# Kernel optimization log

Hardware: AMD Instinct MI355X
Metric: run time of the kernel (lower is better)

Reference implementation:

```python
import jax, jax.numpy as jnp
import numpy as np

B, T, D, U = 32, 2048, 128, 128


def setup_inputs() -> dict:
    key = jax.random.key(0)
    k1, k2, k3, k4 = jax.random.split(key, 4)
    x = jax.random.normal(k1, (B, T, D), dtype=jnp.float32)
    W_x = jax.random.normal(k2, (D, 4 * U), dtype=jnp.float32) * 0.05
    W_h = jax.random.normal(k3, (U, 4 * U), dtype=jnp.float32) * 0.05
    bias = jax.random.normal(k4, (4 * U,), dtype=jnp.float32) * 0.05
    return {"x": x, "W_x": W_x, "W_h": W_h, "bias": bias}


def reference(x, W_x, W_h, bias):
    # Keras gate order in the packed 4U dim: i, f, c(g), o
    u = W_h.shape[0]
    batch = x.shape[0]
    h0 = jnp.zeros((batch, u), dtype=x.dtype)
    c0 = jnp.zeros((batch, u), dtype=x.dtype)

    def step(carry, x_t):
        h, c = carry
        z = x_t @ W_x + h @ W_h + bias  # [B, 4U], fused 4-gate GEMM
        i = jax.nn.sigmoid(z[:, :u])
        f = jax.nn.sigmoid(z[:, u:2 * u])
        g = jnp.tanh(z[:, 2 * u:3 * u])
        o = jax.nn.sigmoid(z[:, 3 * u:])
        c_new = i * g + f * c
        h_new = o * jnp.tanh(c_new)
        return (h_new, c_new), h_new

    # scan over time: x -> [T, B, D]
    _, hs = jax.lax.scan(step, (h0, c0), jnp.swapaxes(x, 0, 1))
    return hs  # [T, B, U], matches original's np.array(h_sequences)
```

## Files before the change

### kernel.cpp

```cpp
#include <hip/hip_runtime.h>
#include <cstdint>
#include <cstddef>

#define B_ 32
#define T_ 2048
#define D_ 128
#define U_ 128
#define G4_ 512
#define P1_ROWS 32
#define L2E_ 1.4426950408889634f

typedef _Float16 f16x8 __attribute__((ext_vector_type(8)));
typedef _Float16 f16x2 __attribute__((ext_vector_type(2)));
typedef float f32x4 __attribute__((ext_vector_type(4)));

__device__ __forceinline__ void lds_barrier() {
  __builtin_amdgcn_sched_barrier(0);
  asm volatile("s_waitcnt lgkmcnt(0)");
  __builtin_amdgcn_sched_barrier(0);
  __builtin_amdgcn_s_barrier();
  __builtin_amdgcn_sched_barrier(0);
}

__global__ __launch_bounds__(512)
void zx_kernel(const float* __restrict__ x, const float* __restrict__ Wx,
               const float* __restrict__ bias, float* __restrict__ Zx,
               int tbase, int ct) {
  const int j = threadIdx.x;
  const int nt = ct / P1_ROWS;
  const int tblk = blockIdx.x % nt;
  const int b = blockIdx.x / nt;
  const int t0 = tblk * P1_ROWS;
  const float sj = ((j >> 7) == 2) ? (-2.f * L2E_) : (-L2E_);

  __shared__ float xsT[D_ * P1_ROWS];

  const float* xp = x + ((size_t)b * T_ + tbase + t0) * D_;
  {
    int e = j * 8;
    int r = e >> 7;
    int k = e & 127;
    float4 v0 = *(const float4*)(xp + e);
    float4 v1 = *(const float4*)(xp + e + 4);
    xsT[(k + 0) * P1_ROWS + r] = v0.x;
    xsT[(k + 1) * P1_ROWS + r] = v0.y;
    xsT[(k + 2) * P1_ROWS + r] = v0.z;
    xsT[(k + 3) * P1_ROWS + r] = v0.w;
    xsT[(k + 4) * P1_ROWS + r] = v1.x;
    xsT[(k + 5) * P1_ROWS + r] = v1.y;
    xsT[(k + 6) * P1_ROWS + r] = v1.z;
    xsT[(k + 7) * P1_ROWS + r] = v1.w;
  }
  __syncthreads();

  const float bj = bias[j];
  float acc[P1_ROWS];
#pragma unroll
  for (int r = 0; r < P1_ROWS; ++r) acc[r] = bj;

  const float* wp = Wx + j;
  float w = wp[0];
#pragma unroll 2
  for (int k = 0; k < D_; ++k) {
    float wn = (k + 1 < D_) ? wp[(size_t)(k + 1) * G4_] : 0.f;
    const float4* xr = (const float4*)(xsT + k * P1_ROWS);
#pragma unroll
    for (int r4 = 0; r4 < P1_ROWS / 4; ++r4) {
      float4 xv = xr[r4];
      acc[4 * r4 + 0] += xv.x * w;
      acc[4 * r4 + 1] += xv.y * w;
      acc[4 * r4 + 2] += xv.z * w;
      acc[4 * r4 + 3] += xv.w * w;
    }
    w = wn;
  }

  float* zp = Zx + ((size_t)b * G4_ + j) * ct + t0;
#pragma unroll
  for (int q = 0; q < P1_ROWS / 4; ++q)
    ((float4*)zp)[q] = make_float4(sj * acc[4 * q], sj * acc[4 * q + 1],
                                   sj * acc[4 * q + 2], sj * acc[4 * q + 3]);
}

__global__ __launch_bounds__(512)
void lstm_kernel(const float* __restrict__ Zx, const float* __restrict__ Wh,
                 float* __restrict__ out, float* __restrict__ state,
                 int tbase, int ct, int first) {
  const int j = threadIdx.x;
  const int b = blockIdx.x;
  const int w = j >> 6;
  const int lane = j & 63;
  const int l4 = lane & 15;
  const int kg = lane >> 4;
  const int u = w * 16 + l4;

  const bool evn = (kg & 1) == 0;
  const bool lowg = kg < 2;
  const int idx16 = (lane ^ 16) << 2;
  const int idx32 = (lane ^ 32) << 2;
  const float mk = (kg == 2) ? 2.f : 1.f;
  const float bk = (kg == 2) ? -1.f : 0.f;

  f16x8 bf[4][4];
#pragma unroll
  for (int g = 0; g < 4; ++g) {
    const float sg = (g == 2) ? (-2.f * L2E_) : (-L2E_);
#pragma unroll
    for (int kt = 0; kt < 4; ++kt) {
      f16x8 v;
#pragma unroll
      for (int e = 0; e < 8; ++e)
        v[e] = (_Float16)(sg * Wh[(size_t)(kt * 32 + kg * 8 + e) * G4_ + g * U_ + u]);
      bf[g][kt] = v;
    }
  }

  __shared__ alignas(16) _Float16 hbuf[2][U_];

  float c_state = 0.f, h0 = 0.f;
  if (!first) {
    h0 = state[b * 2 * U_ + u];
    c_state = state[b * 2 * U_ + U_ + u];
  }
  if (kg == 0) hbuf[0][u] = (_Float16)h0;
  __syncthreads();

  const float4* zq = (const float4*)(Zx + ((size_t)b * G4_ + kg * U_ + u) * ct);
  float4 zc = zq[0];
  float hlast = h0;
  float* outp = out + ((size_t)tbase * B_ + b) * U_ + u;

  const f32x4 zero4 = {0.f, 0.f, 0.f, 0.f};

  for (int tt = 0; tt < ct; tt += 4) {
    float4 zn = (tt + 4 < ct) ? zq[(tt >> 2) + 1] : make_float4(0.f, 0.f, 0.f, 0.f);
#pragma unroll
    for (int s = 0; s < 4; ++s) {
      const int t = tt + s;
      const int cur = t & 1;
      const float zi = (s == 0) ? zc.x : (s == 1) ? zc.y : (s == 2) ? zc.z : zc.w;

      const f16x8* hp = (const f16x8*)hbuf[cur];
      f16x8 a0 = hp[0 * 4 + kg];
      f16x8 a1 = hp[1 * 4 + kg];
      f16x8 a2 = hp[2 * 4 + kg];
      f16x8 a3 = hp[3 * 4 + kg];

      f32x4 c00 = __builtin_amdgcn_mfma_f32_16x16x32_f16(a0, bf[0][0], zero4, 0, 0, 0);
      f32x4 c10 = __builtin_amdgcn_mfma_f32_16x16x32_f16(a0, bf[1][0], zero4, 0, 0, 0);
      f32x4 c20 = __builtin_amdgcn_mfma_f32_16x16x32_f16(a0, bf[2][0], zero4, 0, 0, 0);
      f32x4 c30 = __builtin_amdgcn_mfma_f32_16x16x32_f16(a0, bf[3][0], zero4, 0, 0, 0);
      f32x4 c01 = __builtin_amdgcn_mfma_f32_16x16x32_f16(a1, bf[0][1], zero4, 0, 0, 0);
      f32x4 c11 = __builtin_amdgcn_mfma_f32_16x16x32_f16(a1, bf[1][1], zero4, 0, 0, 0);
      f32x4 c21 = __builtin_amdgcn_mfma_f32_16x16x32_f16(a1, bf[2][1], zero4, 0, 0, 0);
      f32x4 c31 = __builtin_amdgcn_mfma_f32_16x16x32_f16(a1, bf[3][1], zero4, 0, 0, 0);
      f32x4 c02 = __builtin_amdgcn_mfma_f32_16x16x32_f16(a2, bf[0][2], zero4, 0, 0, 0);
      f32x4 c12 = __builtin_amdgcn_mfma_f32_16x16x32_f16(a2, bf[1][2], zero4, 0, 0, 0);
      f32x4 c22 = __builtin_amdgcn_mfma_f32_16x16x32_f16(a2, bf[2][2], zero4, 0, 0, 0);
      f32x4 c32 = __builtin_amdgcn_mfma_f32_16x16x32_f16(a2, bf[3][2], zero4, 0, 0, 0);
      f32x4 c03 = __builtin_amdgcn_mfma_f32_16x16x32_f16(a3, bf[0][3], zero4, 0, 0, 0);
      f32x4 c13 = __builtin_amdgcn_mfma_f32_16x16x32_f16(a3, bf[1][3], zero4, 0, 0, 0);
      f32x4 c23 = __builtin_amdgcn_mfma_f32_16x16x32_f16(a3, bf[2][3], zero4, 0, 0, 0);
      f32x4 c33 = __builtin_amdgcn_mfma_f32_16x16x32_f16(a3, bf[3][3], zero4, 0, 0, 0);

      float z0 = (c00[0] + c01[0]) + (c02[0] + c03[0]);
      float z1 = (c10[0] + c11[0]) + (c12[0] + c13[0]);
      float z2 = (c20[0] + c21[0]) + (c22[0] + c23[0]);
      float z3 = (c30[0] + c31[0]) + (c32[0] + c33[0]);
      float zsel = lowg ? (evn ? z0 : z1) : (evn ? z2 : z3);
      float zs = zsel + zi;

      float act = fmaf(__builtin_amdgcn_rcpf(1.f + __builtin_amdgcn_exp2f(zs)), mk, bk);

      float prt = __builtin_bit_cast(
          float, __builtin_amdgcn_ds_bpermute(idx16, __builtin_bit_cast(int, act)));
      f16x2 spv = __builtin_bit_cast(f16x2, __builtin_amdgcn_cvt_pkrtz(act, prt));
      int oth = __builtin_amdgcn_ds_bpermute(idx32, __builtin_bit_cast(int, spv));
      f16x2 opv = __builtin_bit_cast(f16x2, oth);

      float spl = (float)spv[0], sph = (float)spv[1];
      float opl = (float)opv[0], oph = (float)opv[1];
      float ifl = lowg ? spl : opl, ifh = lowg ? sph : oph;
      float gol = lowg ? opl : spl, goh = lowg ? oph : sph;
      float i_ = evn ? ifl : ifh, f_ = evn ? ifh : ifl;
      float g_ = evn ? gol : goh, o_ = evn ? goh : gol;

      c_state = fmaf(f_, c_state, i_ * g_);
      float tc = fmaf(
          __builtin_amdgcn_rcpf(1.f + __builtin_amdgcn_exp2f(-2.f * L2E_ * c_state)),
          2.f, -1.f);
      float hn = o_ * tc;
      hlast = hn;

      if (kg == 0) {
        outp[(size_t)t * B_ * U_] = hn;
        hbuf[cur ^ 1][u] = (_Float16)hn;
      }
      lds_barrier();
    }
    zc = zn;
  }

  if (kg == 0) {
    state[b * 2 * U_ + u] = hlast;
    state[b * 2 * U_ + U_ + u] = c_state;
  }
}

extern "C" void kernel_launch(void* const* d_in, const int* in_sizes, int n_in,
                              void* d_out, int out_size, void* d_ws, size_t ws_size,
                              hipStream_t stream) {
  const float* x = (const float*)d_in[0];
  const float* Wx = (const float*)d_in[1];
  const float* Wh = (const float*)d_in[2];
  const float* bias = (const float*)d_in[3];
  float* out = (float*)d_out;

  float* state = (float*)d_ws;
  float* zx = (float*)((char*)d_ws + 32768);
  size_t avail = ws_size > 32768 ? ws_size - 32768 : 0;
  size_t per_t = (size_t)B_ * G4_ * sizeof(float);
  long maxct = (long)(avail / per_t);
  int ct;
  if (maxct >= T_) ct = T_;
  else {
    ct = (int)((maxct / P1_ROWS) * P1_ROWS);
    if (ct < P1_ROWS) ct = P1_ROWS;
  }

  for (int tb = 0; tb < T_; tb += ct) {
    int cur = (T_ - tb < ct) ? (T_ - tb) : ct;
    zx_kernel<<<dim3(B_ * (cur / P1_ROWS)), 512, 0, stream>>>(x, Wx, bias, zx, tb, cur);
    lstm_kernel<<<dim3(B_), 512, 0, stream>>>(zx, Wh, out, state, tb, cur, tb == 0 ? 1 : 0);
  }
}
```

Baseline: 1.227 ms.

## Halve LSTM block to 4 waves with each lane computing all gates redundantly

```diff
diff --git a/kernel.cpp b/kernel.cpp
--- a/kernel.cpp
+++ b/kernel.cpp
@@ -11,7 +11,6 @@
 #define L2E_ 1.4426950408889634f
 
 typedef _Float16 f16x8 __attribute__((ext_vector_type(8)));
-typedef _Float16 f16x2 __attribute__((ext_vector_type(2)));
 typedef float f32x4 __attribute__((ext_vector_type(4)));
 
 __device__ __forceinline__ void lds_barrier() {
@@ -82,7 +81,7 @@
                                    sj * acc[4 * q + 2], sj * acc[4 * q + 3]);
 }
 
-__global__ __launch_bounds__(512)
+__global__ __launch_bounds__(256, 1)
 void lstm_kernel(const float* __restrict__ Zx, const float* __restrict__ Wh,
                  float* __restrict__ out, float* __restrict__ state,
                  int tbase, int ct, int first) {
@@ -92,53 +91,70 @@
   const int lane = j & 63;
   const int l4 = lane & 15;
   const int kg = lane >> 4;
-  const int u = w * 16 + l4;
-
-  const bool evn = (kg & 1) == 0;
-  const bool lowg = kg < 2;
-  const int idx16 = (lane ^ 16) << 2;
-  const int idx32 = (lane ^ 32) << 2;
-  const float mk = (kg == 2) ? 2.f : 1.f;
-  const float bk = (kg == 2) ? -1.f : 0.f;
-
-  f16x8 bf[4][4];
+  const int u0 = 32 * w + l4;
+  const int u1 = u0 + 16;
+  const int uo = (kg == 1) ? u1 : u0;
+
+  f16x8 bf[4][2][4];
 #pragma unroll
   for (int g = 0; g < 4; ++g) {
     const float sg = (g == 2) ? (-2.f * L2E_) : (-L2E_);
 #pragma unroll
-    for (int kt = 0; kt < 4; ++kt) {
-      f16x8 v;
-#pragma unroll
-      for (int e = 0; e < 8; ++e)
-        v[e] = (_Float16)(sg * Wh[(size_t)(kt * 32 + kg * 8 + e) * G4_ + g * U_ + u]);
-      bf[g][kt] = v;
+    for (int e = 0; e < 2; ++e) {
+#pragma unroll
+      for (int kt = 0; kt < 4; ++kt) {
+        f16x8 v;
+#pragma unroll
+        for (int el = 0; el < 8; ++el)
+          v[el] = (_Float16)(sg * Wh[(size_t)(kt * 32 + kg * 8 + el) * G4_ +
+                                     g * U_ + 32 * w + 16 * e + l4]);
+        bf[g][e][kt] = v;
+      }
     }
   }
 
   __shared__ alignas(16) _Float16 hbuf[2][U_];
 
-  float c_state = 0.f, h0 = 0.f;
+  float c0s = 0.f, c1s = 0.f, hl0 = 0.f, hl1 = 0.f;
   if (!first) {
-    h0 = state[b * 2 * U_ + u];
-    c_state = state[b * 2 * U_ + U_ + u];
-  }
-  if (kg == 0) hbuf[0][u] = (_Float16)h0;
+    hl0 = state[b * 2 * U_ + u0];
+    hl1 = state[b * 2 * U_ + u1];
+    c0s = state[b * 2 * U_ + U_ + u0];
+    c1s = state[b * 2 * U_ + U_ + u1];
+  }
+  if (lane < 32) hbuf[0][uo] = (_Float16)((kg == 1) ? hl1 : hl0);
   __syncthreads();
 
-  const float4* zq = (const float4*)(Zx + ((size_t)b * G4_ + kg * U_ + u) * ct);
-  float4 zc = zq[0];
-  float hlast = h0;
-  float* outp = out + ((size_t)tbase * B_ + b) * U_ + u;
-
+  const float2* zq[4][2];
+#pragma unroll
+  for (int g = 0; g < 4; ++g)
+#pragma unroll
+    for (int e = 0; e < 2; ++e)
+      zq[g][e] = (const float2*)(Zx + ((size_t)b * G4_ + g * U_ + 32 * w +
+                                       16 * e + l4) * ct);
+
+  float2 zc[4][2], zn[4][2];
+#pragma unroll
+  for (int g = 0; g < 4; ++g)
+#pragma unroll
+    for (int e = 0; e < 2; ++e) zc[g][e] = zq[g][e][0];
+
+  float* outp = out + ((size_t)tbase * B_ + b) * U_ + uo;
   const f32x4 zero4 = {0.f, 0.f, 0.f, 0.f};
 
-  for (int tt = 0; tt < ct; tt += 4) {
-    float4 zn = (tt + 4 < ct) ? zq[(tt >> 2) + 1] : make_float4(0.f, 0.f, 0.f, 0.f);
-#pragma unroll
-    for (int s = 0; s < 4; ++s) {
+  for (int tt = 0; tt < ct; tt += 2) {
+    const bool more = (tt + 2 < ct);
+    const int nq = (tt >> 1) + 1;
+#pragma unroll
+    for (int g = 0; g < 4; ++g)
+#pragma unroll
+      for (int e = 0; e < 2; ++e)
+        zn[g][e] = more ? zq[g][e][nq] : make_float2(0.f, 0.f);
+
+#pragma unroll
+    for (int s = 0; s < 2; ++s) {
       const int t = tt + s;
       const int cur = t & 1;
-      const float zi = (s == 0) ? zc.x : (s == 1) ? zc.y : (s == 2) ? zc.z : zc.w;
 
       const f16x8* hp = (const f16x8*)hbuf[cur];
       f16x8 a0 = hp[0 * 4 + kg];
@@ -146,64 +162,66 @@
       f16x8 a2 = hp[2 * 4 + kg];
       f16x8 a3 = hp[3 * 4 + kg];
 
-      f32x4 c00 = __builtin_amdgcn_mfma_f32_16x16x32_f16(a0, bf[0][0], zero4, 0, 0, 0);
-      f32x4 c10 = __builtin_amdgcn_mfma_f32_16x16x32_f16(a0, bf[1][0], zero4, 0, 0, 0);
-      f32x4 c20 = __builtin_amdgcn_mfma_f32_16x16x32_f16(a0, bf[2][0], zero4, 0, 0, 0);
-      f32x4 c30 = __builtin_amdgcn_mfma_f32_16x16x32_f16(a0, bf[3][0], zero4, 0, 0, 0);
-      f32x4 c01 = __builtin_amdgcn_mfma_f32_16x16x32_f16(a1, bf[0][1], zero4, 0, 0, 0);
-      f32x4 c11 = __builtin_amdgcn_mfma_f32_16x16x32_f16(a1, bf[1][1], zero4, 0, 0, 0);
-      f32x4 c21 = __builtin_amdgcn_mfma_f32_16x16x32_f16(a1, bf[2][1], zero4, 0, 0, 0);
-      f32x4 c31 = __builtin_amdgcn_mfma_f32_16x16x32_f16(a1, bf[3][1], zero4, 0, 0, 0);
-      f32x4 c02 = __builtin_amdgcn_mfma_f32_16x16x32_f16(a2, bf[0][2], zero4, 0, 0, 0);
-      f32x4 c12 = __builtin_amdgcn_mfma_f32_16x16x32_f16(a2, bf[1][2], zero4, 0, 0, 0);
-      f32x4 c22 = __builtin_amdgcn_mfma_f32_16x16x32_f16(a2, bf[2][2], zero4, 0, 0, 0);
-      f32x4 c32 = __builtin_amdgcn_mfma_f32_16x16x32_f16(a2, bf[3][2], zero4, 0, 0, 0);
-      f32x4 c03 = __builtin_amdgcn_mfma_f32_16x16x32_f16(a3, bf[0][3], zero4, 0, 0, 0);
-      f32x4 c13 = __builtin_amdgcn_mfma_f32_16x16x32_f16(a3, bf[1][3], zero4, 0, 0, 0);
-      f32x4 c23 = __builtin_amdgcn_mfma_f32_16x16x32_f16(a3, bf[2][3], zero4, 0, 0, 0);
-      f32x4 c33 = __builtin_amdgcn_mfma_f32_16x16x32_f16(a3, bf[3][3], zero4, 0, 0, 0);
-
-      float z0 = (c00[0] + c01[0]) + (c02[0] + c03[0]);
-      float z1 = (c10[0] + c11[0]) + (c12[0] + c13[0]);
-      float z2 = (c20[0] + c21[0]) + (c22[0] + c23[0]);
-      float z3 = (c30[0] + c31[0]) + (c32[0] + c33[0]);
-      float zsel = lowg ? (evn ? z0 : z1) : (evn ? z2 : z3);
-      float zs = zsel + zi;
-
-      float act = fmaf(__builtin_amdgcn_rcpf(1.f + __builtin_amdgcn_exp2f(zs)), mk, bk);
-
-      float prt = __builtin_bit_cast(
-          float, __builtin_amdgcn_ds_bpermute(idx16, __builtin_bit_cast(int, act)));
-      f16x2 spv = __builtin_bit_cast(f16x2, __builtin_amdgcn_cvt_pkrtz(act, prt));
-      int oth = __builtin_amdgcn_ds_bpermute(idx32, __builtin_bit_cast(int, spv));
-      f16x2 opv = __builtin_bit_cast(f16x2, oth);
-
-      float spl = (float)spv[0], sph = (float)spv[1];
-      float opl = (float)opv[0], oph = (float)opv[1];
-      float ifl = lowg ? spl : opl, ifh = lowg ? sph : oph;
-      float gol = lowg ? opl : spl, goh = lowg ? oph : sph;
-      float i_ = evn ? ifl : ifh, f_ = evn ? ifh : ifl;
-      float g_ = evn ? gol : goh, o_ = evn ? goh : gol;
-
-      c_state = fmaf(f_, c_state, i_ * g_);
-      float tc = fmaf(
-          __builtin_amdgcn_rcpf(1.f + __builtin_amdgcn_exp2f(-2.f * L2E_ * c_state)),
-          2.f, -1.f);
-      float hn = o_ * tc;
-      hlast = hn;
-
-      if (kg == 0) {
-        outp[(size_t)t * B_ * U_] = hn;
-        hbuf[cur ^ 1][u] = (_Float16)hn;
+      f32x4 acc[4][2];
+#pragma unroll
+      for (int g = 0; g < 4; ++g)
+#pragma unroll
+        for (int e = 0; e < 2; ++e)
+          acc[g][e] = __builtin_amdgcn_mfma_f32_16x16x32_f16(a0, bf[g][e][0], zero4, 0, 0, 0);
+#pragma unroll
+      for (int g = 0; g < 4; ++g)
+#pragma unroll
+        for (int e = 0; e < 2; ++e)
+          acc[g][e] = __builtin_amdgcn_mfma_f32_16x16x32_f16(a1, bf[g][e][1], acc[g][e], 0, 0, 0);
+#pragma unroll
+      for (int g = 0; g < 4; ++g)
+#pragma unroll
+        for (int e = 0; e < 2; ++e)
+          acc[g][e] = __builtin_amdgcn_mfma_f32_16x16x32_f16(a2, bf[g][e][2], acc[g][e], 0, 0, 0);
+#pragma unroll
+      for (int g = 0; g < 4; ++g)
+#pragma unroll
+        for (int e = 0; e < 2; ++e)
+          acc[g][e] = __builtin_amdgcn_mfma_f32_16x16x32_f16(a3, bf[g][e][3], acc[g][e], 0, 0, 0);
+
+      float act[4][2];
+#pragma unroll
+      for (int g = 0; g < 4; ++g) {
+        const float mk = (g == 2) ? 2.f : 1.f;
+        const float bk = (g == 2) ? -1.f : 0.f;
+#pragma unroll
+        for (int e = 0; e < 2; ++e) {
+          float zi = (s == 0) ? zc[g][e].x : zc[g][e].y;
+          float zs = acc[g][e][0] + zi;
+          act[g][e] = fmaf(__builtin_amdgcn_rcpf(1.f + __builtin_amdgcn_exp2f(zs)), mk, bk);
+        }
+      }
+
+      c0s = fmaf(act[1][0], c0s, act[0][0] * act[2][0]);
+      c1s = fmaf(act[1][1], c1s, act[0][1] * act[2][1]);
+      float th0 = fmaf(
+          __builtin_amdgcn_rcpf(1.f + __builtin_amdgcn_exp2f(-2.f * L2E_ * c0s)), 2.f, -1.f);
+      float th1 = fmaf(
+          __builtin_amdgcn_rcpf(1.f + __builtin_amdgcn_exp2f(-2.f * L2E_ * c1s)), 2.f, -1.f);
+      hl0 = act[3][0] * th0;
+      hl1 = act[3][1] * th1;
+
+      if (lane < 32) {
+        float hsel = (kg == 1) ? hl1 : hl0;
+        outp[(size_t)t * B_ * U_] = hsel;
+        hbuf[cur ^ 1][uo] = (_Float16)hsel;
       }
       lds_barrier();
     }
-    zc = zn;
-  }
-
-  if (kg == 0) {
-    state[b * 2 * U_ + u] = hlast;
-    state[b * 2 * U_ + U_ + u] = c_state;
+#pragma unroll
+    for (int g = 0; g < 4; ++g)
+#pragma unroll
+      for (int e = 0; e < 2; ++e) zc[g][e] = zn[g][e];
+  }
+
+  if (lane < 32) {
+    state[b * 2 * U_ + uo] = (kg == 1) ? hl1 : hl0;
+    state[b * 2 * U_ + U_ + uo] = (kg == 1) ? c1s : c0s;
   }
 }
 
@@ -231,6 +249,6 @@
   for (int tb = 0; tb < T_; tb += ct) {
     int cur = (T_ - tb < ct) ? (T_ - tb) : ct;
     zx_kernel<<<dim3(B_ * (cur / P1_ROWS)), 512, 0, stream>>>(x, Wx, bias, zx, tb, cur);
-    lstm_kernel<<<dim3(B_), 512, 0, stream>>>(zx, Wh, out, state, tb, cur, tb == 0 ? 1 : 0);
-  }
-}
+    lstm_kernel<<<dim3(B_), 256, 0, stream>>>(zx, Wh, out, state, tb, cur, tb == 0 ? 1 : 0);
+  }
+}
```

After: 1.936 ms. 57.8% more time.
